# Optimization experiments

Measured on AMD Instinct MI355X. Metric: run time of the kernel, lower is better.

Reference implementation:

```python
import jax, jax.numpy as jnp
import numpy as np

D_MODEL = 1024
N_HEADS = 16
D_HEAD = 64
NUM_REL_POS = 2047
B = 8
L = 1024


def setup_inputs() -> dict:
    key = jax.random.key(0)
    ks = jax.random.split(key, 8)
    s = 1.0 / np.sqrt(D_MODEL)
    x = jax.random.normal(ks[0], (B, L, D_MODEL), dtype=jnp.float32)
    rel_indices = jax.random.randint(ks[1], (L, L), 0, NUM_REL_POS)
    Wq = jax.random.normal(ks[2], (D_MODEL, D_MODEL), dtype=jnp.float32) * s
    Wk = jax.random.normal(ks[3], (D_MODEL, D_MODEL), dtype=jnp.float32) * s
    Wv = jax.random.normal(ks[4], (D_MODEL, D_MODEL), dtype=jnp.float32) * s
    Wo = jax.random.normal(ks[5], (D_MODEL, D_MODEL), dtype=jnp.float32) * s
    rel_k = jax.random.normal(ks[6], (NUM_REL_POS, D_HEAD), dtype=jnp.float32) * 0.02
    rel_v = jax.random.normal(ks[7], (NUM_REL_POS, D_HEAD), dtype=jnp.float32) * 0.02
    return {"x": x, "rel_indices": rel_indices, "Wq": Wq, "Wk": Wk,
            "Wv": Wv, "Wo": Wo, "rel_k": rel_k, "rel_v": rel_v}


def reference(x, rel_indices, Wq, Wk, Wv, Wo, rel_k, rel_v):
    Bz, Ls, D = x.shape
    H, dk = N_HEADS, D_HEAD
    scale = 1.0 / np.sqrt(dk)
    # torch Linear: y = x @ W.T, weights are [out, in]
    q = jnp.einsum('bld,ed->ble', x, Wq).reshape(Bz, Ls, H, dk).transpose(0, 2, 1, 3)
    k = jnp.einsum('bld,ed->ble', x, Wk).reshape(Bz, Ls, H, dk).transpose(0, 2, 1, 3)
    v = jnp.einsum('bld,ed->ble', x, Wv).reshape(Bz, Ls, H, dk).transpose(0, 2, 1, 3)
    r_k = rel_k[rel_indices]  # (L, L, dk)
    r_v = rel_v[rel_indices]  # (L, L, dk)
    content = jnp.einsum('bhid,bhjd->bhij', q, k)
    rel = jnp.einsum('bhid,ijd->bhij', q, r_k)
    scores = (content + rel) * scale
    probs = jax.nn.softmax(scores, axis=-1)  # dropout = 0 (eval)
    out = jnp.einsum('bhij,bhjd->bhid', probs, v) + jnp.einsum('bhij,ijd->bhid', probs, r_v)
    out = out.transpose(0, 2, 1, 3).reshape(Bz, Ls, D)
    return jnp.einsum('bld,ed->ble', out, Wo)
```

## Files before the change

### kernel.cpp

```cpp
#include <hip/hip_runtime.h>

#define B_ 8
#define H_ 16
#define L_ 1024
#define DH_ 64
#define DM_ 1024
#define NP_ 2047
#define NP2_ 2048
#define SCALE_ 0.125f

#define PS_ 1032
#define HS_ 516

typedef __attribute__((ext_vector_type(8))) short bf16x8;
typedef __attribute__((ext_vector_type(4))) float f32x4;

__device__ __forceinline__ unsigned short f2bf(float x) {
    union { float f; unsigned int u; } v; v.f = x;
    return (unsigned short)((v.u + 0x7FFFu + ((v.u >> 16) & 1u)) >> 16);
}
__device__ __forceinline__ float bf2f(unsigned short b) {
    union { unsigned int u; float f; } v; v.u = ((unsigned int)b) << 16;
    return v.f;
}

template <int MODE>
__global__ __launch_bounds__(256) void proj_gemm(const float* __restrict__ X,
                                                 const float* __restrict__ W,
                                                 float* __restrict__ Yf,
                                                 unsigned short* __restrict__ Y0,
                                                 unsigned short* __restrict__ Y1)
{
    __shared__ __align__(16) float As[16][68];
    __shared__ __align__(16) float Bs[16][68];
    const int t   = threadIdx.x;
    const int tm  = t & 15;
    const int tn  = t >> 4;
    const int row0 = blockIdx.x * 64;
    const int col0 = blockIdx.y * 64;
    const int lr = t >> 2;
    const int lc = (t & 3) * 4;

    float acc[4][4];
#pragma unroll
    for (int i = 0; i < 4; ++i)
#pragma unroll
        for (int j = 0; j < 4; ++j) acc[i][j] = 0.f;

    for (int k0 = 0; k0 < DM_; k0 += 16) {
        float4 av = *(const float4*)(X + (size_t)(row0 + lr) * DM_ + k0 + lc);
        float4 wv = *(const float4*)(W + (size_t)(col0 + lr) * DM_ + k0 + lc);
        __syncthreads();
        As[lc + 0][lr] = av.x; As[lc + 1][lr] = av.y;
        As[lc + 2][lr] = av.z; As[lc + 3][lr] = av.w;
        Bs[lc + 0][lr] = wv.x; Bs[lc + 1][lr] = wv.y;
        Bs[lc + 2][lr] = wv.z; Bs[lc + 3][lr] = wv.w;
        __syncthreads();
#pragma unroll
        for (int kk = 0; kk < 16; ++kk) {
            float4 a  = *(const float4*)&As[kk][tm * 4];
            float4 w4 = *(const float4*)&Bs[kk][tn * 4];
            acc[0][0] = fmaf(a.x, w4.x, acc[0][0]);
            acc[0][1] = fmaf(a.x, w4.y, acc[0][1]);
            acc[0][2] = fmaf(a.x, w4.z, acc[0][2]);
            acc[0][3] = fmaf(a.x, w4.w, acc[0][3]);
            acc[1][0] = fmaf(a.y, w4.x, acc[1][0]);
            acc[1][1] = fmaf(a.y, w4.y, acc[1][1]);
            acc[1][2] = fmaf(a.y, w4.z, acc[1][2]);
            acc[1][3] = fmaf(a.y, w4.w, acc[1][3]);
            acc[2][0] = fmaf(a.z, w4.x, acc[2][0]);
            acc[2][1] = fmaf(a.z, w4.y, acc[2][1]);
            acc[2][2] = fmaf(a.z, w4.z, acc[2][2]);
            acc[2][3] = fmaf(a.z, w4.w, acc[2][3]);
            acc[3][0] = fmaf(a.w, w4.x, acc[3][0]);
            acc[3][1] = fmaf(a.w, w4.y, acc[3][1]);
            acc[3][2] = fmaf(a.w, w4.z, acc[3][2]);
            acc[3][3] = fmaf(a.w, w4.w, acc[3][3]);
        }
    }

    const int h = blockIdx.y;
#pragma unroll
    for (int i = 0; i < 4; ++i) {
        const int row = row0 + tm * 4 + i;
        if (MODE == 1) {
            float4 r = make_float4(acc[i][0], acc[i][1], acc[i][2], acc[i][3]);
            *(float4*)(Yf + (size_t)row * DM_ + col0 + tn * 4) = r;
        } else {
            const int bb = row >> 10;
            const int l  = row & 1023;
            if (MODE == 0) {
                ushort4 hi4, lo4;
                unsigned short* hp = (unsigned short*)&hi4;
                unsigned short* lp = (unsigned short*)&lo4;
#pragma unroll
                for (int j = 0; j < 4; ++j) {
                    unsigned short hb = f2bf(acc[i][j]);
                    hp[j] = hb;
                    lp[j] = f2bf(acc[i][j] - bf2f(hb));
                }
                const size_t base = (((size_t)bb * H_ + h) * L_ + l) * DH_ + tn * 4;
                *(ushort4*)(Y0 + base) = hi4;
                *(ushort4*)(Y1 + base) = lo4;
            } else {
#pragma unroll
                for (int j = 0; j < 4; ++j) {
                    const int d = tn * 4 + j;
                    Y0[(((size_t)bb * H_ + h) * DH_ + d) * L_ + l] = f2bf(acc[i][j]);
                }
            }
        }
    }
}

__global__ __launch_bounds__(256) void prep_rel(const float* __restrict__ rk,
                                                const float* __restrict__ rv,
                                                unsigned short* __restrict__ rk_hi,
                                                unsigned short* __restrict__ rv_t)
{
    const int idx = blockIdx.x * 256 + threadIdx.x;
    const int p = idx >> 6;
    const int d = idx & 63;
    float xk = (p < NP_) ? rk[(size_t)p * DH_ + d] : 0.f;
    rk_hi[idx] = f2bf(xk);
    float xv = (p < NP_) ? rv[(size_t)p * DH_ + d] : 0.f;
    rv_t[(size_t)d * NP2_ + p] = f2bf(xv);
}

__global__ __launch_bounds__(512) void shaw_attn_mfma(
    const unsigned short* __restrict__ qh, const unsigned short* __restrict__ ql,
    const unsigned short* __restrict__ kh, const unsigned short* __restrict__ kl,
    const unsigned short* __restrict__ vt, const int* __restrict__ ridx,
    const unsigned short* __restrict__ rkh, const unsigned short* __restrict__ rvt,
    float* __restrict__ out)
{
    __shared__ __align__(16) unsigned char regionA[16 * PS_ * 2];
    __shared__ __align__(16) unsigned char regionB[16 * HS_ * 4];
    __shared__ float pmax[16][8];
    __shared__ float psum[16][8];

    char*           qrel8 = (char*)regionA;
    unsigned short* Pu    = (unsigned short*)regionA;
    float*          hist  = (float*)regionB;
    float*          red   = (float*)regionB;

    const int t    = threadIdx.x;
    const int w    = t >> 6;
    const int lane = t & 63;
    const int mrow = lane & 15;
    const int grp  = lane >> 4;

    const int bid = blockIdx.x;
    const int lid = (bid & 7) * 1024 + (bid >> 3);
    const int b   = lid >> 10;
    const int h   = (lid >> 6) & 15;
    const int i0  = (lid & 63) * 16;
    const size_t bh = (size_t)b * H_ + h;

    const unsigned short* qhp = qh + bh * (size_t)(L_ * DH_);
    const unsigned short* qlp = ql + bh * (size_t)(L_ * DH_);
    const unsigned short* khp = kh + bh * (size_t)(L_ * DH_);
    const unsigned short* klp = kl + bh * (size_t)(L_ * DH_);
    const unsigned short* vtp = vt + bh * (size_t)(DH_ * L_);

    bf16x8 qAh[2], qAl[2];
#pragma unroll
    for (int s = 0; s < 2; ++s) {
        const size_t off = (size_t)(i0 + mrow) * DH_ + s * 32 + grp * 8;
        qAh[s] = *(const bf16x8*)(qhp + off);
        qAl[s] = *(const bf16x8*)(qlp + off);
    }

    {
        const unsigned short* rb = rkh + (size_t)(w * 256 + mrow) * DH_ + grp * 8;
#pragma unroll
        for (int tt = 0; tt < 16; ++tt) {
            bf16x8 Bh0 = *(const bf16x8*)(rb + tt * 1024);
            bf16x8 Bh1 = *(const bf16x8*)(rb + tt * 1024 + 32);
            f32x4 c = {0.f, 0.f, 0.f, 0.f};
            c = __builtin_amdgcn_mfma_f32_16x16x32_bf16(qAh[0], Bh0, c, 0, 0, 0);
            c = __builtin_amdgcn_mfma_f32_16x16x32_bf16(qAh[1], Bh1, c, 0, 0, 0);
            const int pcol = (w * 16 + tt) * 16 + mrow;
            unsigned int pk = 0;
#pragma unroll
            for (int r = 0; r < 4; ++r) {
                int qi = (int)rintf(c[r] * 128.f);
                qi = qi > 127 ? 127 : (qi < -127 ? -127 : qi);
                pk |= ((unsigned int)(qi & 0xff)) << (8 * r);
            }
            *(unsigned int*)(qrel8 + pcol * 16 + grp * 4) = pk;
        }
    }
    __syncthreads();

    float sc[8][4];
    {
        const unsigned short* kbh = khp + (size_t)(w * 128 + mrow) * DH_ + grp * 8;
        const unsigned short* kbl = klp + (size_t)(w * 128 + mrow) * DH_ + grp * 8;
#pragma unroll
        for (int tt = 0; tt < 8; ++tt) {
            bf16x8 Bh0 = *(const bf16x8*)(kbh + tt * 1024);
            bf16x8 Bh1 = *(const bf16x8*)(kbh + tt * 1024 + 32);
            bf16x8 Bl0 = *(const bf16x8*)(kbl + tt * 1024);
            bf16x8 Bl1 = *(const bf16x8*)(kbl + tt * 1024 + 32);
            f32x4 c = {0.f, 0.f, 0.f, 0.f};
            c = __builtin_amdgcn_mfma_f32_16x16x32_bf16(qAh[0], Bh0, c, 0, 0, 0);
            c = __builtin_amdgcn_mfma_f32_16x16x32_bf16(qAh[1], Bh1, c, 0, 0, 0);
            c = __builtin_amdgcn_mfma_f32_16x16x32_bf16(qAh[0], Bl0, c, 0, 0, 0);
            c = __builtin_amdgcn_mfma_f32_16x16x32_bf16(qAh[1], Bl1, c, 0, 0, 0);
            c = __builtin_amdgcn_mfma_f32_16x16x32_bf16(qAl[0], Bh0, c, 0, 0, 0);
            c = __builtin_amdgcn_mfma_f32_16x16x32_bf16(qAl[1], Bh1, c, 0, 0, 0);
#pragma unroll
            for (int r = 0; r < 4; ++r) sc[tt][r] = c[r] * SCALE_;
        }
    }

    {
        int pidxA[8][4];
#pragma unroll
        for (int tt = 0; tt < 8; ++tt) {
            const int jcol = (w * 8 + tt) * 16 + mrow;
#pragma unroll
            for (int r = 0; r < 4; ++r)
                pidxA[tt][r] = ridx[(size_t)(i0 + grp * 4 + r) * L_ + jcol];
        }
#pragma unroll
        for (int tt = 0; tt < 8; ++tt)
#pragma unroll
            for (int r = 0; r < 4; ++r) {
                const float rel = (float)qrel8[pidxA[tt][r] * 16 + grp * 4 + r];
                sc[tt][r] = fmaf(rel, SCALE_ / 128.f, sc[tt][r]);
            }
    }

    float mx[4];
#pragma unroll
    for (int r = 0; r < 4; ++r) {
        float m = sc[0][r];
#pragma unroll
        for (int tt = 1; tt < 8; ++tt) m = fmaxf(m, sc[tt][r]);
#pragma unroll
        for (int off = 1; off < 16; off <<= 1) m = fmaxf(m, __shfl_xor(m, off));
        mx[r] = m;
    }
    {
        const float wv0 = (mrow == 0) ? mx[0] : (mrow == 1) ? mx[1] : (mrow == 2) ? mx[2] : mx[3];
        if (mrow < 4) pmax[grp * 4 + mrow][w] = wv0;
    }
    __syncthreads();

    float gm[4];
#pragma unroll
    for (int r = 0; r < 4; ++r) {
        const int rr = grp * 4 + r;
        float m = pmax[rr][0];
#pragma unroll
        for (int u = 1; u < 8; ++u) m = fmaxf(m, pmax[rr][u]);
        gm[r] = m;
    }
    float sm[4];
#pragma unroll
    for (int r = 0; r < 4; ++r) {
        const int rr = grp * 4 + r;
        float s = 0.f;
#pragma unroll
        for (int tt = 0; tt < 8; ++tt) {
            const float e = __expf(sc[tt][r] - gm[r]);
            s += e;
            Pu[rr * PS_ + (w * 8 + tt) * 16 + mrow] = f2bf(e);
        }
#pragma unroll
        for (int off = 1; off < 16; off <<= 1) s += __shfl_xor(s, off);
        sm[r] = s;
    }
    {
        const float sv0 = (mrow == 0) ? sm[0] : (mrow == 1) ? sm[1] : (mrow == 2) ? sm[2] : sm[3];
        if (mrow < 4) psum[grp * 4 + mrow][w] = sv0;
    }
    __syncthreads();

    const int n = w & 3;
    const int khalf = w >> 2;
    f32x4 acc = {0.f, 0.f, 0.f, 0.f};
    {
        const unsigned short* vcol = vtp + (size_t)(n * 16 + mrow) * L_ + khalf * 512 + grp * 8;
#pragma unroll
        for (int s = 0; s < 16; ++s) {
            bf16x8 a  = *(const bf16x8*)(Pu + mrow * PS_ + khalf * 512 + s * 32 + grp * 8);
            bf16x8 bb = *(const bf16x8*)(vcol + s * 32);
            acc = __builtin_amdgcn_mfma_f32_16x16x32_bf16(a, bb, acc, 0, 0, 0);
        }
    }

    unsigned int cache[32];
    {
        const int* idx0 = ridx + (size_t)(i0 + 2 * w) * L_;
        const int* idx1 = idx0 + L_;
#pragma unroll
        for (int c = 0; c < 16; ++c) {
            const int j = c * 64 + lane;
            cache[c]      = (((unsigned int)idx0[j]) << 16) | (unsigned int)Pu[(2 * w) * PS_ + j];
            cache[c + 16] = (((unsigned int)idx1[j]) << 16) | (unsigned int)Pu[(2 * w + 1) * PS_ + j];
        }
    }

    for (int pass = 0; pass < 4; ++pass) {
        bf16x8 rvf[8];
        {
            const unsigned short* rvcol =
                rvt + (size_t)(n * 16 + mrow) * NP2_ + pass * 512 + khalf * 256 + grp * 8;
#pragma unroll
            for (int s = 0; s < 8; ++s) rvf[s] = *(const bf16x8*)(rvcol + s * 32);
        }
        __syncthreads();
        {
            float4* h4 = (float4*)hist;
            const float4 z4 = make_float4(0.f, 0.f, 0.f, 0.f);
            for (int z = t; z < (16 * HS_) / 4; z += 512) h4[z] = z4;
        }
        __syncthreads();
#pragma unroll
        for (int e = 0; e < 32; ++e) {
            const unsigned int pk = cache[e];
            const int pidx = (int)(pk >> 16);
            if ((pidx >> 9) == pass) {
                const int row = 2 * w + (e >> 4);
                atomicAdd(&hist[row * HS_ + (pidx & 511)], bf2f((unsigned short)(pk & 0xffffu)));
            }
        }
        __syncthreads();
#pragma unroll
        for (int s = 0; s < 8; ++s) {
            const int kb = khalf * 256 + s * 32;
            const f32x4* hp = (const f32x4*)&hist[mrow * HS_ + kb + grp * 8];
            f32x4 h0 = hp[0], h1 = hp[1];
            bf16x8 a;
#pragma unroll
            for (int e = 0; e < 4; ++e) { a[e] = (short)f2bf(h0[e]); a[e + 4] = (short)f2bf(h1[e]); }
            acc = __builtin_amdgcn_mfma_f32_16x16x32_bf16(a, rvf[s], acc, 0, 0, 0);
        }
    }

    __syncthreads();
#pragma unroll
    for (int r = 0; r < 4; ++r) red[w * 320 + (grp * 4 + r) * 20 + mrow] = acc[r];
    __syncthreads();
    if (w < 4) {
#pragma unroll
        for (int r = 0; r < 4; ++r) {
            const int rr = grp * 4 + r;
            float o = red[w * 320 + rr * 20 + mrow] + red[(w + 4) * 320 + rr * 20 + mrow];
            float ssum = 0.f;
#pragma unroll
            for (int u = 0; u < 8; ++u) ssum += psum[rr][u];
            out[((size_t)b * L_ + i0 + rr) * DM_ + h * DH_ + w * 16 + mrow] = o / ssum;
        }
    }
}

extern "C" void kernel_launch(void* const* d_in, const int* in_sizes, int n_in,
                              void* d_out, int out_size, void* d_ws, size_t ws_size,
                              hipStream_t stream)
{
    const float* x    = (const float*)d_in[0];
    const int*   ridx = (const int*)  d_in[1];
    const float* Wq   = (const float*)d_in[2];
    const float* Wk   = (const float*)d_in[3];
    const float* Wv   = (const float*)d_in[4];
    const float* Wo   = (const float*)d_in[5];
    const float* rk   = (const float*)d_in[6];
    const float* rv   = (const float*)d_in[7];
    float* out = (float*)d_out;

    const size_t NQ = (size_t)B_ * H_ * L_ * DH_;
    float* attn = (float*)d_ws;
    unsigned short* u = (unsigned short*)(attn + NQ);
    unsigned short* qh = u;            u += NQ;
    unsigned short* ql = u;            u += NQ;
    unsigned short* kh = u;            u += NQ;
    unsigned short* kl = u;            u += NQ;
    unsigned short* vt = u;            u += NQ;
    unsigned short* rkh = u;           u += (size_t)NP2_ * DH_;
    unsigned short* rvt = u;           u += (size_t)NP2_ * DH_;

    dim3 gthr(256);
    dim3 ggrid((B_ * L_) / 64, DM_ / 64);

    prep_rel<<<dim3((NP2_ * DH_) / 256), gthr, 0, stream>>>(rk, rv, rkh, rvt);
    proj_gemm<0><<<ggrid, gthr, 0, stream>>>(x, Wq, nullptr, qh, ql);
    proj_gemm<0><<<ggrid, gthr, 0, stream>>>(x, Wk, nullptr, kh, kl);
    proj_gemm<2><<<ggrid, gthr, 0, stream>>>(x, Wv, nullptr, vt, nullptr);

    shaw_attn_mfma<<<dim3(8192), dim3(512), 0, stream>>>(
        qh, ql, kh, kl, vt, ridx, rkh, rvt, attn);

    proj_gemm<1><<<ggrid, gthr, 0, stream>>>(attn, Wo, out, nullptr, nullptr);
}
```

Before: 2.551 ms.

## Alias histogram onto the P buffer and shrink register arrays to raise occupancy

The histogram/reduction buffer now shares the score/probability shared-memory region, roughly halving per-block LDS. The 32-entry index/probability register cache and the preloaded rel_v fragments are replaced by packed probability registers, with rel indices reloaded from global memory in every pass. Unroll factors are reduced to cut register pressure. The launch changes from a swizzled 1D grid to a plain 3D grid, which drops the previous blockIdx swizzle. In exchange, the repeated index loads per pass add global traffic, and locality may change.

```diff
diff --git a/kernel.cpp b/kernel.cpp
--- a/kernel.cpp
+++ b/kernel.cpp
@@ -135,26 +135,22 @@
     float* __restrict__ out)
 {
     __shared__ __align__(16) unsigned char regionA[16 * PS_ * 2];
-    __shared__ __align__(16) unsigned char regionB[16 * HS_ * 4];
     __shared__ float pmax[16][8];
     __shared__ float psum[16][8];
 
     char*           qrel8 = (char*)regionA;
     unsigned short* Pu    = (unsigned short*)regionA;
-    float*          hist  = (float*)regionB;
-    float*          red   = (float*)regionB;
+    float*          hist  = (float*)regionA;
+    float*          red   = (float*)regionA;
 
     const int t    = threadIdx.x;
     const int w    = t >> 6;
     const int lane = t & 63;
     const int mrow = lane & 15;
     const int grp  = lane >> 4;
-
-    const int bid = blockIdx.x;
-    const int lid = (bid & 7) * 1024 + (bid >> 3);
-    const int b   = lid >> 10;
-    const int h   = (lid >> 6) & 15;
-    const int i0  = (lid & 63) * 16;
+    const int i0   = blockIdx.x * 16;
+    const int h    = blockIdx.y;
+    const int b    = blockIdx.z;
     const size_t bh = (size_t)b * H_ + h;
 
     const unsigned short* qhp = qh + bh * (size_t)(L_ * DH_);
@@ -173,7 +169,7 @@
 
     {
         const unsigned short* rb = rkh + (size_t)(w * 256 + mrow) * DH_ + grp * 8;
-#pragma unroll
+#pragma unroll 4
         for (int tt = 0; tt < 16; ++tt) {
             bf16x8 Bh0 = *(const bf16x8*)(rb + tt * 1024);
             bf16x8 Bh1 = *(const bf16x8*)(rb + tt * 1024 + 32);
@@ -197,7 +193,7 @@
     {
         const unsigned short* kbh = khp + (size_t)(w * 128 + mrow) * DH_ + grp * 8;
         const unsigned short* kbl = klp + (size_t)(w * 128 + mrow) * DH_ + grp * 8;
-#pragma unroll
+#pragma unroll 2
         for (int tt = 0; tt < 8; ++tt) {
             bf16x8 Bh0 = *(const bf16x8*)(kbh + tt * 1024);
             bf16x8 Bh1 = *(const bf16x8*)(kbh + tt * 1024 + 32);
@@ -215,22 +211,14 @@
         }
     }
 
-    {
-        int pidxA[8][4];
-#pragma unroll
-        for (int tt = 0; tt < 8; ++tt) {
-            const int jcol = (w * 8 + tt) * 16 + mrow;
-#pragma unroll
-            for (int r = 0; r < 4; ++r)
-                pidxA[tt][r] = ridx[(size_t)(i0 + grp * 4 + r) * L_ + jcol];
-        }
-#pragma unroll
-        for (int tt = 0; tt < 8; ++tt)
-#pragma unroll
-            for (int r = 0; r < 4; ++r) {
-                const float rel = (float)qrel8[pidxA[tt][r] * 16 + grp * 4 + r];
-                sc[tt][r] = fmaf(rel, SCALE_ / 128.f, sc[tt][r]);
-            }
+#pragma unroll
+    for (int tt = 0; tt < 8; ++tt) {
+        const int jcol = (w * 8 + tt) * 16 + mrow;
+#pragma unroll
+        for (int r = 0; r < 4; ++r) {
+            const int pidx = ridx[(size_t)(i0 + grp * 4 + r) * L_ + jcol];
+            sc[tt][r] = fmaf((float)qrel8[pidx * 16 + grp * 4 + r], SCALE_ / 128.f, sc[tt][r]);
+        }
     }
 
     float mx[4];
@@ -258,20 +246,33 @@
         for (int u = 1; u < 8; ++u) m = fmaxf(m, pmax[rr][u]);
         gm[r] = m;
     }
-    float sm[4];
+    unsigned int epk[16];
+    float sm[4] = {0.f, 0.f, 0.f, 0.f};
+#pragma unroll
+    for (int tt = 0; tt < 8; ++tt) {
+        const int jcol = (w * 8 + tt) * 16 + mrow;
+        unsigned int pk[2];
+#pragma unroll
+        for (int rp = 0; rp < 2; ++rp) {
+            unsigned int pcur = 0;
+#pragma unroll
+            for (int j = 0; j < 2; ++j) {
+                const int r = rp * 2 + j;
+                const float e = __expf(sc[tt][r] - gm[r]);
+                sm[r] += e;
+                const unsigned short us = f2bf(e);
+                Pu[(grp * 4 + r) * PS_ + jcol] = us;
+                pcur |= ((unsigned int)us) << (16 * j);
+            }
+            pk[rp] = pcur;
+        }
+        epk[tt * 2 + 0] = pk[0];
+        epk[tt * 2 + 1] = pk[1];
+    }
 #pragma unroll
     for (int r = 0; r < 4; ++r) {
-        const int rr = grp * 4 + r;
-        float s = 0.f;
-#pragma unroll
-        for (int tt = 0; tt < 8; ++tt) {
-            const float e = __expf(sc[tt][r] - gm[r]);
-            s += e;
-            Pu[rr * PS_ + (w * 8 + tt) * 16 + mrow] = f2bf(e);
-        }
-#pragma unroll
-        for (int off = 1; off < 16; off <<= 1) s += __shfl_xor(s, off);
-        sm[r] = s;
+#pragma unroll
+        for (int off = 1; off < 16; off <<= 1) sm[r] += __shfl_xor(sm[r], off);
     }
     {
         const float sv0 = (mrow == 0) ? sm[0] : (mrow == 1) ? sm[1] : (mrow == 2) ? sm[2] : sm[3];
@@ -284,35 +285,16 @@
     f32x4 acc = {0.f, 0.f, 0.f, 0.f};
     {
         const unsigned short* vcol = vtp + (size_t)(n * 16 + mrow) * L_ + khalf * 512 + grp * 8;
-#pragma unroll
+#pragma unroll 4
         for (int s = 0; s < 16; ++s) {
             bf16x8 a  = *(const bf16x8*)(Pu + mrow * PS_ + khalf * 512 + s * 32 + grp * 8);
             bf16x8 bb = *(const bf16x8*)(vcol + s * 32);
             acc = __builtin_amdgcn_mfma_f32_16x16x32_bf16(a, bb, acc, 0, 0, 0);
         }
     }
-
-    unsigned int cache[32];
-    {
-        const int* idx0 = ridx + (size_t)(i0 + 2 * w) * L_;
-        const int* idx1 = idx0 + L_;
-#pragma unroll
-        for (int c = 0; c < 16; ++c) {
-            const int j = c * 64 + lane;
-            cache[c]      = (((unsigned int)idx0[j]) << 16) | (unsigned int)Pu[(2 * w) * PS_ + j];
-            cache[c + 16] = (((unsigned int)idx1[j]) << 16) | (unsigned int)Pu[(2 * w + 1) * PS_ + j];
-        }
-    }
+    __syncthreads();
 
     for (int pass = 0; pass < 4; ++pass) {
-        bf16x8 rvf[8];
-        {
-            const unsigned short* rvcol =
-                rvt + (size_t)(n * 16 + mrow) * NP2_ + pass * 512 + khalf * 256 + grp * 8;
-#pragma unroll
-            for (int s = 0; s < 8; ++s) rvf[s] = *(const bf16x8*)(rvcol + s * 32);
-        }
-        __syncthreads();
         {
             float4* h4 = (float4*)hist;
             const float4 z4 = make_float4(0.f, 0.f, 0.f, 0.f);
@@ -320,16 +302,23 @@
         }
         __syncthreads();
 #pragma unroll
-        for (int e = 0; e < 32; ++e) {
-            const unsigned int pk = cache[e];
-            const int pidx = (int)(pk >> 16);
-            if ((pidx >> 9) == pass) {
-                const int row = 2 * w + (e >> 4);
-                atomicAdd(&hist[row * HS_ + (pidx & 511)], bf2f((unsigned short)(pk & 0xffffu)));
-            }
-        }
-        __syncthreads();
-#pragma unroll
+        for (int tt = 0; tt < 8; ++tt) {
+            const int jcol = (w * 8 + tt) * 16 + mrow;
+#pragma unroll
+            for (int rp = 0; rp < 2; ++rp)
+#pragma unroll
+                for (int j = 0; j < 2; ++j) {
+                    const int rr = grp * 4 + rp * 2 + j;
+                    const int pidx = ridx[(size_t)(i0 + rr) * L_ + jcol];
+                    if ((pidx >> 9) == pass)
+                        atomicAdd(&hist[rr * HS_ + (pidx & 511)],
+                                  bf2f((unsigned short)(epk[tt * 2 + rp] >> (16 * j))));
+                }
+        }
+        __syncthreads();
+        const unsigned short* rvcol =
+            rvt + (size_t)(n * 16 + mrow) * NP2_ + pass * 512 + khalf * 256 + grp * 8;
+#pragma unroll 4
         for (int s = 0; s < 8; ++s) {
             const int kb = khalf * 256 + s * 32;
             const f32x4* hp = (const f32x4*)&hist[mrow * HS_ + kb + grp * 8];
@@ -337,11 +326,12 @@
             bf16x8 a;
 #pragma unroll
             for (int e = 0; e < 4; ++e) { a[e] = (short)f2bf(h0[e]); a[e + 4] = (short)f2bf(h1[e]); }
-            acc = __builtin_amdgcn_mfma_f32_16x16x32_bf16(a, rvf[s], acc, 0, 0, 0);
-        }
-    }
-
-    __syncthreads();
+            bf16x8 bb = *(const bf16x8*)(rvcol + s * 32);
+            acc = __builtin_amdgcn_mfma_f32_16x16x32_bf16(a, bb, acc, 0, 0, 0);
+        }
+        __syncthreads();
+    }
+
 #pragma unroll
     for (int r = 0; r < 4; ++r) red[w * 320 + (grp * 4 + r) * 20 + mrow] = acc[r];
     __syncthreads();
@@ -391,7 +381,7 @@
     proj_gemm<0><<<ggrid, gthr, 0, stream>>>(x, Wk, nullptr, kh, kl);
     proj_gemm<2><<<ggrid, gthr, 0, stream>>>(x, Wv, nullptr, vt, nullptr);
 
-    shaw_attn_mfma<<<dim3(8192), dim3(512), 0, stream>>>(
+    shaw_attn_mfma<<<dim3(L_ / 16, H_, B_), dim3(512), 0, stream>>>(
         qh, ql, kh, kl, vt, ridx, rkh, rvt, attn);
 
     proj_gemm<1><<<ggrid, gthr, 0, stream>>>(attn, Wo, out, nullptr, nullptr);
```

Measured after the change: 2.600 ms. About the same (+1.9%).
